# Kernel optimization log

Hardware: AMD Instinct MI355X
Metric: run time of the kernel (lower is better)

Reference implementation:

```python
import jax, jax.numpy as jnp
import numpy as np
import math

NHEAD = 8
IOU_THR = 0.2
COS_THR = 0.2


def _build_mask(segments, q):
    # segments: [bz, Lq, 2] (center, length); q: [bz, Lq, d]
    c, l = segments[..., 0], segments[..., 1]
    s, e = c - l / 2, c + l / 2  # ml2se: midpoint-length -> start-end
    inter = jnp.clip(jnp.minimum(e[:, :, None], e[:, None, :])
                     - jnp.maximum(s[:, :, None], s[:, None, :]), 0.0)
    union = l[:, :, None] + l[:, None, :] - inter
    iou = inter / union  # [bz, Lq, Lq]
    qn = q / jnp.maximum(jnp.linalg.norm(q, axis=-1, keepdims=True), 1e-8)
    cos = jnp.einsum('bid,bjd->bij', qn, qn)
    Lq = q.shape[1]
    adj = jnp.broadcast_to(jnp.eye(Lq, dtype=bool), iou.shape)
    adj = jnp.where(iou <= IOU_THR, True, adj)   # adj_matrix[iou<=0.2]=1
    adj = jnp.where(cos <= COS_THR, False, adj)  # adj_matrix[cos<=0.2]=0
    return ~adj  # True = masked


def setup_inputs() -> dict:
    key = jax.random.key(0)
    ks = jax.random.split(key, 8)
    Lq, bz, d = 1024, 8, 512
    bound = 1.0 / math.sqrt(d)
    query = jax.random.normal(ks[0], (Lq, bz, d), jnp.float32)
    segments = jax.random.uniform(ks[1], (bz, Lq, 2), jnp.float32)
    Wq = jax.random.uniform(ks[2], (d, d), jnp.float32, -bound, bound)
    bq = jax.random.uniform(ks[3], (d,), jnp.float32, -bound, bound)
    Wk = jax.random.uniform(ks[4], (d, d), jnp.float32, -bound, bound)
    bk = jax.random.uniform(ks[5], (d,), jnp.float32, -bound, bound)
    Wv = jax.random.uniform(ks[6], (d, d), jnp.float32, -bound, bound)
    bv = jax.random.uniform(ks[7], (d,), jnp.float32, -bound, bound)
    return dict(query=query, segments=segments, Wq=Wq, bq=bq, Wk=Wk, bk=bk,
                Wv=Wv, bv=bv)


def reference(query, segments, Wq, bq, Wk, bk, Wv, bv):
    Lq, bz, d = query.shape
    dh = d // NHEAD
    h = jnp.transpose(query, (1, 0, 2))  # [bz, Lq, d]
    mask = _build_mask(segments, h)      # [bz, Lq, Lq], bool
    Q = (h @ Wq.T + bq).reshape(bz, Lq, NHEAD, dh)
    K = (h @ Wk.T + bk).reshape(bz, Lq, NHEAD, dh)
    V = (h @ Wv.T + bv).reshape(bz, Lq, NHEAD, dh)
    scores = jnp.einsum('bihd,bjhd->bhij', Q, K) / math.sqrt(dh)
    scores = jnp.where(mask[:, None, :, :], -jnp.inf, scores)
    attn = jax.nn.softmax(scores, axis=-1)
    out = jnp.einsum('bhij,bjhd->bihd', attn, V).reshape(bz, Lq, d) + h
    return jnp.transpose(out, (1, 0, 2))  # [Lq, bz, d]
```

## Files before the change

kernel.cpp:

```cpp
#include <hip/hip_runtime.h>
#include <math.h>

#define LQ 1024
#define BZ 8
#define D  512
#define NH 8
#define DH 64
#define IOU_THR 0.2f
#define COS_THR 0.2f
#define NEG (-1e30f)
#define FIXCAP 16384

typedef short bf16x8 __attribute__((ext_vector_type(8)));
typedef float f32x4  __attribute__((ext_vector_type(4)));

#define MFMA16(a, b, cacc) __builtin_amdgcn_mfma_f32_16x16x32_bf16(a, b, cacc, 0, 0, 0)

__device__ inline unsigned short f2bf(float x) {
    union { float f; unsigned int u; } v; v.f = x;
    unsigned int r = v.u + 0x7FFF + ((v.u >> 16) & 1);
    return (unsigned short)(r >> 16);
}

__device__ __forceinline__ void gll16(const void* g, void* ldsbase) {
    __builtin_amdgcn_global_load_lds(
        (const __attribute__((address_space(1))) unsigned int*)g,
        (__attribute__((address_space(3))) unsigned int*)ldsbase, 16, 0, 0);
}

__global__ __launch_bounds__(256) void prep_kernel(const float* __restrict__ query,
                                                   const float* __restrict__ Wq,
                                                   const float* __restrict__ Wk,
                                                   const float* __restrict__ Wv,
                                                   unsigned short* __restrict__ hi,
                                                   unsigned short* __restrict__ Wb,
                                                   float* __restrict__ rnorm) {
    int blk = blockIdx.x, tid = threadIdx.x;
    if (blk < 2048) {
        int w = tid >> 6, lane = tid & 63;
        int row = blk * 4 + w;
        int b = row >> 10, i = row & 1023;
        const float* src = query + ((size_t)i * BZ + b) * D + lane * 8;
        float4 v0 = *(const float4*)src;
        float4 v1 = *(const float4*)(src + 4);
        uint4 pk;
        pk.x = (unsigned)f2bf(v0.x) | ((unsigned)f2bf(v0.y) << 16);
        pk.y = (unsigned)f2bf(v0.z) | ((unsigned)f2bf(v0.w) << 16);
        pk.z = (unsigned)f2bf(v1.x) | ((unsigned)f2bf(v1.y) << 16);
        pk.w = (unsigned)f2bf(v1.z) | ((unsigned)f2bf(v1.w) << 16);
        *(uint4*)(hi + (size_t)row * D + lane * 8) = pk;
        float ss = v0.x * v0.x + v0.y * v0.y + v0.z * v0.z + v0.w * v0.w
                 + v1.x * v1.x + v1.y * v1.y + v1.z * v1.z + v1.w * v1.w;
        #pragma unroll
        for (int s = 1; s < 64; s <<= 1) ss += __shfl_xor(ss, s);
        if (lane == 0) rnorm[row] = 1.0f / fmaxf(sqrtf(ss), 1e-8f);
    } else {
        int t = (blk - 2048) * 256 + tid;
        int mat = t >> 16;
        int off = (t & 65535) * 4;
        const float* src = (mat == 0) ? Wq : (mat == 1) ? Wk : Wv;
        float4 v = *(const float4*)(src + off);
        uint2 p;
        p.x = (unsigned)f2bf(v.x) | ((unsigned)f2bf(v.y) << 16);
        p.y = (unsigned)f2bf(v.z) | ((unsigned)f2bf(v.w) << 16);
        *(uint2*)(Wb + (size_t)mat * D * D + off) = p;
    }
}

__global__ __launch_bounds__(256) void gemm_kernel(const unsigned short* __restrict__ hi,
                                                   const unsigned short* __restrict__ Wb,
                                                   const float* __restrict__ rnorm,
                                                   const float* __restrict__ segments,
                                                   const float* __restrict__ bq,
                                                   const float* __restrict__ bk,
                                                   const float* __restrict__ bv,
                                                   unsigned char* __restrict__ mask,
                                                   unsigned char* __restrict__ summ,
                                                   int* __restrict__ fix_cnt,
                                                   unsigned int* __restrict__ fix_list,
                                                   unsigned short* __restrict__ Qb,
                                                   unsigned short* __restrict__ Kb,
                                                   unsigned short* __restrict__ Vt) {
    __shared__ short As[128 * 64], Bs[128 * 64];
    __shared__ float4 iSE[128], jSE[128];
    __shared__ int summ_lds[8][2], summ_t_lds[8][2];
    int blk = blockIdx.x, tid = threadIdx.x, w = tid >> 6, lane = tid & 63;
    int c = lane & 15, q4 = lane >> 4;
    int wr = w >> 1, wc = w & 1;

    bool is_qkv = blk < 768;
    const char *Asrc, *Bsrc;
    int b = 0, i0 = 0, j0 = 0, z = 0, m0 = 0, n0 = 0;
    if (is_qkv) {
        z = blk >> 8; int rem = blk & 255;
        m0 = (rem >> 2) * 128; n0 = (rem & 3) * 128;
        Asrc = (const char*)(hi + (size_t)m0 * D);
        Bsrc = (const char*)(Wb + (size_t)z * D * D + (size_t)n0 * D);
    } else {
        int id2 = blk - 768;
        b = id2 / 36;
        int t = id2 - b * 36;
        int it = 0;
        while (t >= 8 - it) { t -= 8 - it; it++; }
        int jt = it + t;
        i0 = it * 128; j0 = jt * 128;
        Asrc = (const char*)(hi + ((size_t)b * LQ + i0) * D);
        Bsrc = (const char*)(hi + ((size_t)b * LQ + j0) * D);
        if (tid < 16) {
            summ_lds[tid >> 1][tid & 1] = 0;
            summ_t_lds[tid >> 1][tid & 1] = 0;
        }
    }

    int rgrp = lane >> 3;
    int qg   = (lane & 7) ^ (rgrp & 7);
    size_t lgoff = (size_t)rgrp * 1024 + (size_t)qg * 16;
    int swz = c & 7;

    f32x4 acc[4][4] = {};
    for (int k0 = 0; k0 < D; k0 += 64) {
        size_t kb = (size_t)k0 * 2;
        #pragma unroll
        for (int m = 0; m < 4; m++) {
            int n = 4 * w + m;
            gll16(Asrc + kb + (size_t)n * 8192 + lgoff, (char*)As + n * 1024);
            gll16(Bsrc + kb + (size_t)n * 8192 + lgoff, (char*)Bs + n * 1024);
        }
        __syncthreads();
        #pragma unroll
        for (int s = 0; s < 2; s++) {
            bf16x8 af[4], bf[4];
            #pragma unroll
            for (int f = 0; f < 4; f++) {
                af[f] = *(const bf16x8*)&As[(wr * 64 + f * 16 + c) * 64 + ((s * 4 + q4) ^ swz) * 8];
                bf[f] = *(const bf16x8*)&Bs[(wc * 64 + f * 16 + c) * 64 + ((s * 4 + q4) ^ swz) * 8];
            }
            #pragma unroll
            for (int fr = 0; fr < 4; fr++)
                #pragma unroll
                for (int fc = 0; fc < 4; fc++)
                    acc[fr][fc] = MFMA16(af[fr], bf[fc], acc[fr][fc]);
        }
        __syncthreads();
    }

    if (is_qkv) {
        const float* bias = (z == 0) ? bq : (z == 1) ? bk : bv;
        #pragma unroll
        for (int fr = 0; fr < 4; fr++)
            #pragma unroll
            for (int r = 0; r < 4; r++) {
                int m = m0 + wr * 64 + fr * 16 + q4 * 4 + r;
                int bb = m >> 10, i = m & 1023;
                #pragma unroll
                for (int fc = 0; fc < 4; fc++) {
                    int n = n0 + wc * 64 + fc * 16 + c;
                    unsigned short us = f2bf(acc[fr][fc][r] + bias[n]);
                    int hh = n >> 6, dh = n & 63;
                    size_t bh = (size_t)bb * NH + hh;
                    if (z == 2)
                        Vt[(bh * DH + dh) * LQ + i] = us;
                    else {
                        unsigned short* dst = (z == 0) ? Qb : Kb;
                        dst[(bh * LQ + i) * DH + dh] = us;
                    }
                }
            }
    } else {
        const float2* seg2 = (const float2*)(segments + (size_t)b * LQ * 2);
        const float* rn = rnorm + b * LQ;
        if (tid < 128) {
            float2 cl = seg2[i0 + tid];
            iSE[tid] = make_float4(cl.x - cl.y * 0.5f, cl.x + cl.y * 0.5f, cl.y, rn[i0 + tid]);
        } else {
            float2 cl = seg2[j0 + tid - 128];
            jSE[tid - 128] = make_float4(cl.x - cl.y * 0.5f, cl.x + cl.y * 0.5f, cl.y, rn[j0 + tid - 128]);
        }
        __syncthreads();

        bool offdiag = (i0 != j0);
        unsigned char* mbase = mask + ((size_t)b << 20);
        int anyT[4] = {0, 0, 0, 0};
        #pragma unroll
        for (int fr = 0; fr < 4; fr++) {
            int anyun = 0;
            unsigned int tpack[4] = {0, 0, 0, 0};
            #pragma unroll
            for (int r = 0; r < 4; r++) {
                int il = wr * 64 + fr * 16 + q4 * 4 + r;
                int i = i0 + il;
                float4 I = iSE[il];
                #pragma unroll
                for (int fc = 0; fc < 4; fc++) {
                    int jl = wc * 64 + fc * 16 + c;
                    int j = j0 + jl;
                    float4 J = jSE[jl];
                    float cosv = acc[fr][fc][r] * I.w * J.w;
                    if (fabsf(cosv - COS_THR) < 1.5e-3f) {
                        int idx = atomicAdd(fix_cnt, 1);
                        if (idx < FIXCAP)
                            fix_list[idx] = ((unsigned int)b << 20) | ((unsigned int)i << 10) | j;
                    }
                    float inter = fmaxf(fminf(I.y, J.y) - fmaxf(I.x, J.x), 0.0f);
                    float uni   = I.z + J.z - inter;
                    float iou   = inter / uni;
                    bool adj = ((iou <= IOU_THR) || (i == j)) && (cosv > COS_THR);
                    mbase[(size_t)i * LQ + j] = adj ? 0 : 1;
                    tpack[fc] |= (adj ? 0u : 1u) << (8 * r);
                    anyun |= adj ? 1 : 0;
                    anyT[fc] |= adj ? 1 : 0;
                }
            }
            if (anyun) atomicOr(&summ_lds[wr * 4 + fr][wc], 1);
            if (offdiag) {
                int ibase = i0 + wr * 64 + fr * 16 + q4 * 4;
                #pragma unroll
                for (int fc = 0; fc < 4; fc++) {
                    int j = j0 + wc * 64 + fc * 16 + c;
                    *(unsigned int*)&mbase[(size_t)j * LQ + ibase] = tpack[fc];
                }
            }
        }
        if (offdiag) {
            #pragma unroll
            for (int fc = 0; fc < 4; fc++)
                if (anyT[fc]) atomicOr(&summ_t_lds[wc * 4 + fc][wr], 1);
        }
        __syncthreads();
        if (tid < 16) {
            int lit = tid >> 1, ljt = tid & 1;
            summ[((size_t)b * 64 + (i0 >> 4) + lit) * 16 + (j0 >> 6) + ljt] =
                summ_lds[lit][ljt] ? 1 : 0;
            if (offdiag)
                summ[((size_t)b * 64 + (j0 >> 4) + lit) * 16 + (i0 >> 6) + ljt] =
                    summ_t_lds[lit][ljt] ? 1 : 0;
        }
    }
}

__global__ __launch_bounds__(64) void fixup_kernel(const float* __restrict__ query,
                                                   const float* __restrict__ rnorm,
                                                   const float* __restrict__ segments,
                                                   const int* __restrict__ fix_cnt,
                                                   const unsigned int* __restrict__ fix_list,
                                                   unsigned char* __restrict__ mask,
                                                   unsigned char* __restrict__ summ) {
    int cnt = *fix_cnt; if (cnt > FIXCAP) cnt = FIXCAP;
    int lane = threadIdx.x;
    for (int e = blockIdx.x; e < cnt; e += gridDim.x) {
        unsigned int pk = fix_list[e];
        int b = pk >> 20, i = (pk >> 10) & 1023, j = pk & 1023;
        const float* hri = query + ((size_t)i * BZ + b) * D;
        const float* hrj = query + ((size_t)j * BZ + b) * D;
        double dd = 0.0;
        #pragma unroll
        for (int k = 0; k < D / 64; k++)
            dd += (double)hri[k * 64 + lane] * (double)hrj[k * 64 + lane];
        #pragma unroll
        for (int s = 1; s < 64; s <<= 1) dd += __shfl_xor(dd, s);
        if (lane == 0) {
            float rni = rnorm[b * LQ + i], rnj = rnorm[b * LQ + j];
            float cosv = (float)(dd * (double)rni * (double)rnj);
            const float* seg = segments + (size_t)b * LQ * 2;
            float ci = seg[i * 2], li = seg[i * 2 + 1];
            float cj = seg[j * 2], lj = seg[j * 2 + 1];
            float si = ci - li * 0.5f, ei = ci + li * 0.5f;
            float sj = cj - lj * 0.5f, ej = cj + lj * 0.5f;
            float inter = fmaxf(fminf(ei, ej) - fmaxf(si, sj), 0.0f);
            float iou = inter / (li + lj - inter);
            bool adj = ((iou <= IOU_THR) || (i == j)) && (cosv > COS_THR);
            unsigned char mv = adj ? 0 : 1;
            mask[((size_t)b * LQ + i) * LQ + j] = mv;
            mask[((size_t)b * LQ + j) * LQ + i] = mv;
            if (adj) {
                summ[((size_t)b * 64 + (i >> 4)) * 16 + (j >> 6)] = 1;
                summ[((size_t)b * 64 + (j >> 4)) * 16 + (i >> 6)] = 1;
            }
        }
    }
}

__global__ __launch_bounds__(256) void attn_kernel(const unsigned short* __restrict__ Qb,
                                                   const unsigned short* __restrict__ Kb,
                                                   const unsigned short* __restrict__ Vt,
                                                   const unsigned char* __restrict__ mask,
                                                   const unsigned char* __restrict__ summ,
                                                   const float* __restrict__ query,
                                                   float* __restrict__ out) {
    int tid = threadIdx.x;
    int w = tid >> 6, lane = tid & 63;
    int c = lane & 15, q4 = lane >> 4;
    int hh = blockIdx.y, b = blockIdx.z;
    int i0 = blockIdx.x * 64 + w * 16;
    size_t bh = (size_t)b * NH + hh;

    __shared__ unsigned short p_lds[4][16][72];

    const unsigned short* Qrow = Qb + (bh * LQ + i0 + c) * DH;
    bf16x8 qa0 = *(const bf16x8*)(Qrow + q4 * 8);
    bf16x8 qa1 = *(const bf16x8*)(Qrow + 32 + q4 * 8);

    f32x4 O[4] = {};
    float m_r[4] = {NEG, NEG, NEG, NEG};
    float l_r[4] = {0.f, 0.f, 0.f, 0.f};

    const unsigned short* Kbase = Kb + bh * LQ * DH;
    const unsigned short* Vbase = Vt + bh * DH * LQ;
    const unsigned char*  mbase = mask + ((size_t)b * LQ + i0) * LQ;
    const unsigned char*  srow  = summ + ((size_t)b * 64 + (i0 >> 4)) * 16;

    for (int jt = 0; jt < 16; jt++) {
        if (!srow[jt]) continue;
        int j0 = jt * 64;
        f32x4 S[4] = {};
        #pragma unroll
        for (int cb = 0; cb < 4; cb++) {
            const unsigned short* krow = Kbase + (size_t)(j0 + cb * 16 + c) * DH;
            bf16x8 kf0 = *(const bf16x8*)(krow + q4 * 8);
            bf16x8 kf1 = *(const bf16x8*)(krow + 32 + q4 * 8);
            S[cb] = MFMA16(qa0, kf0, S[cb]);
            S[cb] = MFMA16(qa1, kf1, S[cb]);
        }
        float p[4][4];
        float tmax[4] = {NEG, NEG, NEG, NEG};
        #pragma unroll
        for (int cb = 0; cb < 4; cb++)
            #pragma unroll
            for (int r = 0; r < 4; r++) {
                float sc = S[cb][r] * 0.125f;
                unsigned char mm = mbase[(size_t)(q4 * 4 + r) * LQ + j0 + cb * 16 + c];
                sc = mm ? NEG : sc;
                p[cb][r] = sc;
                tmax[r] = fmaxf(tmax[r], sc);
            }
        #pragma unroll
        for (int r = 0; r < 4; r++) {
            float v = tmax[r];
            v = fmaxf(v, __shfl_xor(v, 1));
            v = fmaxf(v, __shfl_xor(v, 2));
            v = fmaxf(v, __shfl_xor(v, 4));
            v = fmaxf(v, __shfl_xor(v, 8));
            tmax[r] = v;
        }
        float rsum[4];
        #pragma unroll
        for (int r = 0; r < 4; r++) {
            float mn = fmaxf(m_r[r], tmax[r]);
            float alpha = __expf(m_r[r] - mn);
            m_r[r] = mn;
            l_r[r] *= alpha;
            #pragma unroll
            for (int cb2 = 0; cb2 < 4; cb2++) O[cb2][r] *= alpha;
            float s0 = 0.f;
            #pragma unroll
            for (int cb = 0; cb < 4; cb++) {
                float e = __expf(p[cb][r] - mn);
                p[cb][r] = e;
                s0 += e;
            }
            rsum[r] = s0;
        }
        #pragma unroll
        for (int r = 0; r < 4; r++) {
            float v = rsum[r];
            v += __shfl_xor(v, 1);
            v += __shfl_xor(v, 2);
            v += __shfl_xor(v, 4);
            v += __shfl_xor(v, 8);
            l_r[r] += v;
        }
        #pragma unroll
        for (int cb = 0; cb < 4; cb++)
            #pragma unroll
            for (int r = 0; r < 4; r++)
                p_lds[w][q4 * 4 + r][cb * 16 + c] = f2bf(p[cb][r]);
        #pragma unroll
        for (int s = 0; s < 2; s++) {
            bf16x8 pf = *(const bf16x8*)&p_lds[w][c][s * 32 + q4 * 8];
            #pragma unroll
            for (int cb = 0; cb < 4; cb++) {
                bf16x8 vf = *(const bf16x8*)(Vbase + (size_t)(cb * 16 + c) * LQ + j0 + s * 32 + q4 * 8);
                O[cb] = MFMA16(pf, vf, O[cb]);
            }
        }
    }
    #pragma unroll
    for (int r = 0; r < 4; r++) {
        int i = i0 + q4 * 4 + r;
        float inv = 1.0f / l_r[r];
        #pragma unroll
        for (int cb = 0; cb < 4; cb++) {
            int col = hh * 64 + cb * 16 + c;
            size_t oidx = ((size_t)i * BZ + b) * D + col;
            out[oidx] = O[cb][r] * inv + query[oidx];
        }
    }
}

extern "C" void kernel_launch(void* const* d_in, const int* in_sizes, int n_in,
                              void* d_out, int out_size, void* d_ws, size_t ws_size,
                              hipStream_t stream) {
    const float* query    = (const float*)d_in[0];
    const float* segments = (const float*)d_in[1];
    const float* Wq = (const float*)d_in[2];
    const float* bq = (const float*)d_in[3];
    const float* Wk = (const float*)d_in[4];
    const float* bk = (const float*)d_in[5];
    const float* Wv = (const float*)d_in[6];
    const float* bv = (const float*)d_in[7];
    float* out = (float*)d_out;

    const size_t NTOK = (size_t)BZ * LQ;
    char* ws = (char*)d_ws;
    unsigned short* hbuf  = (unsigned short*)ws;   ws += NTOK * D * 2;
    unsigned short* Qb    = (unsigned short*)ws;   ws += NTOK * D * 2;
    unsigned short* Kb    = (unsigned short*)ws;   ws += NTOK * D * 2;
    unsigned short* Vt    = (unsigned short*)ws;   ws += NTOK * D * 2;
    unsigned short* Wb    = (unsigned short*)ws;   ws += (size_t)3 * D * D * 2;
    float*          rnorm = (float*)ws;            ws += NTOK * 4;
    unsigned char*  mask  = (unsigned char*)ws;    ws += (size_t)BZ * LQ * LQ;
    unsigned char*  summ  = (unsigned char*)ws;    ws += 8192;
    int*            fix_cnt = (int*)ws;            ws += 64;
    unsigned int*   fix_list = (unsigned int*)ws;

    hipMemsetAsync(fix_cnt, 0, 64, stream);
    prep_kernel<<<2816, 256, 0, stream>>>(query, Wq, Wk, Wv, hbuf, Wb, rnorm);
    gemm_kernel<<<1056, 256, 0, stream>>>(hbuf, Wb, rnorm, segments, bq, bk, bv,
                                          mask, summ, fix_cnt, fix_list, Qb, Kb, Vt);
    fixup_kernel<<<64, 64, 0, stream>>>(query, rnorm, segments, fix_cnt, fix_list, mask, summ);
    attn_kernel<<<dim3(LQ / 64, NH, BZ), 256, 0, stream>>>(Qb, Kb, Vt, mask, summ, query, out);
}
```

Baseline: 160.2 us.

## Double-buffer GEMM K-loop with register-staged prefetch and narrower K tile

```diff
diff --git a/kernel.cpp b/kernel.cpp
--- a/kernel.cpp
+++ b/kernel.cpp
@@ -20,12 +20,6 @@
     union { float f; unsigned int u; } v; v.f = x;
     unsigned int r = v.u + 0x7FFF + ((v.u >> 16) & 1);
     return (unsigned short)(r >> 16);
-}
-
-__device__ __forceinline__ void gll16(const void* g, void* ldsbase) {
-    __builtin_amdgcn_global_load_lds(
-        (const __attribute__((address_space(1))) unsigned int*)g,
-        (__attribute__((address_space(3))) unsigned int*)ldsbase, 16, 0, 0);
 }
 
 __global__ __launch_bounds__(256) void prep_kernel(const float* __restrict__ query,
@@ -81,7 +75,7 @@
                                                    unsigned short* __restrict__ Qb,
                                                    unsigned short* __restrict__ Kb,
                                                    unsigned short* __restrict__ Vt) {
-    __shared__ short As[128 * 64], Bs[128 * 64];
+    __shared__ short As[2][128 * 32], Bs[2][128 * 32];
     __shared__ float4 iSE[128], jSE[128];
     __shared__ int summ_lds[8][2], summ_t_lds[8][2];
     int blk = blockIdx.x, tid = threadIdx.x, w = tid >> 6, lane = tid & 63;
@@ -112,34 +106,58 @@
         }
     }
 
-    int rgrp = lane >> 3;
-    int qg   = (lane & 7) ^ (rgrp & 7);
-    size_t lgoff = (size_t)rgrp * 1024 + (size_t)qg * 16;
-    int swz = c & 7;
+    int lrow = lane >> 2;
+    int gl   = (lane & 3) ^ ((lane >> 3) & 3);
+    size_t goff = (size_t)lrow * 1024 + (size_t)gl * 16;
+    int lds_off = lrow * 64 + (lane & 3) * 16;
+
+    uint4 ra[2], rb[2];
+    #pragma unroll
+    for (int m = 0; m < 2; m++) {
+        int n = 2 * w + m;
+        ra[m] = *(const uint4*)(Asrc + (size_t)n * 16384 + goff);
+        rb[m] = *(const uint4*)(Bsrc + (size_t)n * 16384 + goff);
+    }
+    #pragma unroll
+    for (int m = 0; m < 2; m++) {
+        int n = 2 * w + m;
+        *(uint4*)((char*)As[0] + n * 1024 + lds_off) = ra[m];
+        *(uint4*)((char*)Bs[0] + n * 1024 + lds_off) = rb[m];
+    }
+    __syncthreads();
 
     f32x4 acc[4][4] = {};
-    for (int k0 = 0; k0 < D; k0 += 64) {
-        size_t kb = (size_t)k0 * 2;
-        #pragma unroll
-        for (int m = 0; m < 4; m++) {
-            int n = 4 * w + m;
-            gll16(Asrc + kb + (size_t)n * 8192 + lgoff, (char*)As + n * 1024);
-            gll16(Bsrc + kb + (size_t)n * 8192 + lgoff, (char*)Bs + n * 1024);
-        }
-        __syncthreads();
-        #pragma unroll
-        for (int s = 0; s < 2; s++) {
-            bf16x8 af[4], bf[4];
-            #pragma unroll
-            for (int f = 0; f < 4; f++) {
-                af[f] = *(const bf16x8*)&As[(wr * 64 + f * 16 + c) * 64 + ((s * 4 + q4) ^ swz) * 8];
-                bf[f] = *(const bf16x8*)&Bs[(wc * 64 + f * 16 + c) * 64 + ((s * 4 + q4) ^ swz) * 8];
-            }
-            #pragma unroll
-            for (int fr = 0; fr < 4; fr++)
-                #pragma unroll
-                for (int fc = 0; fc < 4; fc++)
-                    acc[fr][fc] = MFMA16(af[fr], bf[fc], acc[fr][fc]);
+    int rswz = (c >> 1) & 3;
+    for (int k = 0; k < 16; k++) {
+        int cur = k & 1;
+        if (k < 15) {
+            size_t kb = (size_t)(k + 1) * 64;
+            #pragma unroll
+            for (int m = 0; m < 2; m++) {
+                int n = 2 * w + m;
+                ra[m] = *(const uint4*)(Asrc + kb + (size_t)n * 16384 + goff);
+                rb[m] = *(const uint4*)(Bsrc + kb + (size_t)n * 16384 + goff);
+            }
+        }
+        bf16x8 af[4], bf[4];
+        #pragma unroll
+        for (int f = 0; f < 4; f++) {
+            af[f] = *(const bf16x8*)&As[cur][(wr * 64 + f * 16 + c) * 32 + (q4 ^ rswz) * 8];
+            bf[f] = *(const bf16x8*)&Bs[cur][(wc * 64 + f * 16 + c) * 32 + (q4 ^ rswz) * 8];
+        }
+        #pragma unroll
+        for (int fr = 0; fr < 4; fr++)
+            #pragma unroll
+            for (int fc = 0; fc < 4; fc++)
+                acc[fr][fc] = MFMA16(af[fr], bf[fc], acc[fr][fc]);
+        if (k < 15) {
+            int nxt = cur ^ 1;
+            #pragma unroll
+            for (int m = 0; m < 2; m++) {
+                int n = 2 * w + m;
+                *(uint4*)((char*)As[nxt] + n * 1024 + lds_off) = ra[m];
+                *(uint4*)((char*)Bs[nxt] + n * 1024 + lds_off) = rb[m];
+            }
         }
         __syncthreads();
     }
```

Result: no change. 159.2 us (-0.6%).
